# Kernel optimization log

Measured on AMD Instinct MI355X. Metric: run time of the kernel, lower is better.

## Reference

```python
import jax, jax.numpy as jnp
import numpy as np

N_HEADS = 16


def setup_inputs() -> dict:
    key = jax.random.key(0)
    k1, k2, k3, k4 = jax.random.split(key, 4)
    B, W, c, C = 4, 1024, 32, 1024
    x = jax.random.normal(k1, (B, W, c, C), dtype=jnp.float32)
    w_pos_emb = jax.random.normal(k2, (W, C), dtype=jnp.float32)
    attn_w = jax.random.normal(k3, (3 * C, C), dtype=jnp.float32) * (1.0 / np.sqrt(C))
    proj_w = jax.random.normal(k4, (C, C), dtype=jnp.float32) * (1.0 / np.sqrt(C))
    attention_mask = jnp.ones((B, W, c), dtype=jnp.int32)
    return {"x": x, "w_pos_emb": w_pos_emb, "attn_w": attn_w,
            "proj_w": proj_w, "attention_mask": attention_mask}


def reference(x, w_pos_emb, attn_w, proj_w, attention_mask):
    B, W, c, C = x.shape
    H = N_HEADS
    Dh = C // H
    # last-token pooling: one-hot of (count-1) over char axis, multiply-sum
    last_ix = attention_mask.sum(-1) - 1                      # [B, W]
    oh = jax.nn.one_hot(last_ix, c, dtype=x.dtype)            # [B, W, c]
    word = jnp.einsum('bwcd,bwc->bwd', x, oh)                 # [B, W, C]
    word = word + w_pos_emb                                   # first_time pos-emb add
    # QKV projection (torch Linear: y = x @ W^T)
    qkv = jnp.einsum('bwd,ed->bwe', word, attn_w)             # [B, W, 3C]
    q, k, v = jnp.split(qkv, 3, axis=-1)
    def heads(t):
        return t.reshape(B, W, H, Dh).transpose(0, 2, 1, 3)   # [B, H, W, Dh]
    q, k, v = heads(q), heads(k), heads(v)
    scale = 1.0 / np.sqrt(Dh).astype(np.float32)
    scores = jnp.einsum('bhqd,bhkd->bhqk', q, k) * scale      # [B, H, W, W]
    causal = jnp.tril(jnp.ones((W, W), dtype=bool))
    scores = jnp.where(causal, scores, jnp.finfo(scores.dtype).min)
    probs = jax.nn.softmax(scores, axis=-1)
    out = jnp.einsum('bhqk,bhkd->bhqd', probs, v)             # [B, H, W, Dh]
    out = out.transpose(0, 2, 1, 3).reshape(B, W, C)
    out = jnp.einsum('bwd,ed->bwe', out, proj_w)              # c_proj
    # dropout is identity in eval mode
    return (word, out)
```

## Files before the change

kernel.cpp:

```cpp
#include <hip/hip_runtime.h>

#define BB 4
#define WW 1024
#define CDIM 1024
#define CCH 32
#define NH 16
#define DH 64
#define MROWS (BB * WW)

typedef __bf16 bf16x8 __attribute__((ext_vector_type(8)));
typedef float f32x4 __attribute__((ext_vector_type(4)));

static __device__ __forceinline__ unsigned short f2bf(float f) {
    union { float f; unsigned u; } v; v.f = f;
    unsigned r = v.u + 0x7fffu + ((v.u >> 16) & 1u);
    return (unsigned short)(r >> 16);
}

#if defined(__has_builtin)
#if __has_builtin(__builtin_amdgcn_global_load_lds)
#define HAVE_GLL 1
#endif
#endif

#ifdef HAVE_GLL
static __device__ __forceinline__ void gload16(const void* g, void* l) {
    __builtin_amdgcn_global_load_lds(
        (const __attribute__((address_space(1))) unsigned int*)g,
        (__attribute__((address_space(3))) unsigned int*)l, 16, 0, 0);
}
#endif

__global__ __launch_bounds__(256) void prep_kernel(const float* __restrict__ aw,
                                                   const float* __restrict__ pw,
                                                   const float* __restrict__ x,
                                                   const float* __restrict__ pos,
                                                   const int* __restrict__ mask,
                                                   unsigned short* __restrict__ awb,
                                                   unsigned short* __restrict__ pwb,
                                                   float* __restrict__ word_f32,
                                                   unsigned short* __restrict__ word_bf) {
    int blk = blockIdx.x;
    if (blk < 4096) {
        int g = blk * 256 + threadIdx.x;
        const int NA4 = 3 * CDIM * CDIM / 4;
        if (g < NA4) {
            float4 vv = ((const float4*)aw)[g];
            ushort4 o = { f2bf(vv.x), f2bf(vv.y), f2bf(vv.z), f2bf(vv.w) };
            ((ushort4*)awb)[g] = o;
        } else {
            int kk = g - NA4;
            float4 vv = ((const float4*)pw)[kk];
            ushort4 o = { f2bf(vv.x), f2bf(vv.y), f2bf(vv.z), f2bf(vv.w) };
            ((ushort4*)pwb)[kk] = o;
        }
    } else {
        int bw = blk - 4096;
        int w = bw & (WW - 1);
        __shared__ int s_last;
        if (threadIdx.x == 0) {
            int ssum = 0;
            for (int j = 0; j < CCH; ++j) ssum += mask[bw * CCH + j];
            s_last = ssum - 1;
        }
        __syncthreads();
        int last = s_last;
        const float4* xr = (const float4*)(x + ((size_t)bw * CCH + (last < 0 ? 0 : last)) * CDIM);
        const float4* pr = (const float4*)(pos + (size_t)w * CDIM);
        int d4 = threadIdx.x;
        float4 xv = (last >= 0) ? xr[d4] : float4{0.f, 0.f, 0.f, 0.f};
        float4 pv = pr[d4];
        float4 vv = { xv.x + pv.x, xv.y + pv.y, xv.z + pv.z, xv.w + pv.w };
        ((float4*)(word_f32 + (size_t)bw * CDIM))[d4] = vv;
        ushort4 o = { f2bf(vv.x), f2bf(vv.y), f2bf(vv.z), f2bf(vv.w) };
        ((ushort4*)(word_bf + (size_t)bw * CDIM))[d4] = o;
    }
}

template <int EPI, int BM, int BN, int WRN, int WCN, int MI, int NI, int NBX, int CW>
__global__ __launch_bounds__(WRN * WCN * 64) void gemm_nt_kernel(
        const unsigned short* __restrict__ A,
        const unsigned short* __restrict__ Bt,
        int Mdim, int Ndim, int Kdim,
        unsigned short* __restrict__ qb,
        unsigned short* __restrict__ kb,
        unsigned short* __restrict__ vb,
        float* __restrict__ outp) {
    const int NW = WRN * WCN;
    const int NT = NW * 64;
    __shared__ unsigned short As[BM * 64];
    __shared__ unsigned short Bs[BN * 64];
    int t = threadIdx.x;
    int wid = t >> 6, lane = t & 63;
    int wr = wid / WCN, wc = wid % WCN;
    int bid = blockIdx.x;
    int xcd = bid & 7, idx = bid >> 3;
    int bx = xcd * CW + idx % CW;
    int by = idx / CW;
    int mbase = by * BM, nbase = bx * BN;
    int lr = lane & 15, lg = lane >> 4;
    f32x4 acc[MI][NI] = {};

#ifdef HAVE_GLL
    int csrc = ((lane & 7) ^ (lane >> 3)) * 8;
    int rofs = lane >> 3;
    const int TOT = (BM + BN) / 8;
#endif

    for (int kt = 0; kt < Kdim; kt += 64) {
        __syncthreads();
#ifdef HAVE_GLL
        for (int cch = wid; cch < TOT; cch += NW) {
            if (cch < BM / 8)
                gload16(A + (size_t)(mbase + cch * 8 + rofs) * Kdim + kt + csrc, &As[cch * 8 * 64]);
            else {
                int cb = cch - BM / 8;
                gload16(Bt + (size_t)(nbase + cb * 8 + rofs) * Kdim + kt + csrc, &Bs[cb * 8 * 64]);
            }
        }
#else
        for (int s = 0; s < (BM + BN) * 8 / NT; ++s) {
            int f = s * NT + t;
            int row = f >> 3, c8 = (f & 7) * 8;
            if (row < BM)
                *(int4*)&As[row * 64 + (c8 ^ ((row & 7) << 3))] =
                    *(const int4*)&A[(size_t)(mbase + row) * Kdim + kt + c8];
            else {
                int rb = row - BM;
                *(int4*)&Bs[rb * 64 + (c8 ^ ((rb & 7) << 3))] =
                    *(const int4*)&Bt[(size_t)(nbase + rb) * Kdim + kt + c8];
            }
        }
#endif
        __syncthreads();
        for (int ks = 0; ks < 2; ++ks) {
            bf16x8 af[MI], bfr[NI];
            int cc = ks * 32 + lg * 8;
            for (int mi = 0; mi < MI; ++mi) {
                int r = wr * (MI * 16) + mi * 16 + lr;
                af[mi] = *(const bf16x8*)&As[r * 64 + (cc ^ ((r & 7) << 3))];
            }
            for (int ni = 0; ni < NI; ++ni) {
                int r = wc * (NI * 16) + ni * 16 + lr;
                bfr[ni] = *(const bf16x8*)&Bs[r * 64 + (cc ^ ((r & 7) << 3))];
            }
            __builtin_amdgcn_s_setprio(1);
            for (int mi = 0; mi < MI; ++mi)
                for (int ni = 0; ni < NI; ++ni)
                    acc[mi][ni] = __builtin_amdgcn_mfma_f32_16x16x32_bf16(af[mi], bfr[ni], acc[mi][ni], 0, 0, 0);
            __builtin_amdgcn_s_setprio(0);
        }
    }
    for (int mi = 0; mi < MI; ++mi)
        for (int ni = 0; ni < NI; ++ni)
            for (int i = 0; i < 4; ++i) {
                int row = mbase + wr * (MI * 16) + mi * 16 + lg * 4 + i;
                int col = nbase + wc * (NI * 16) + ni * 16 + lr;
                float v = acc[mi][ni][i];
                if (EPI == 0) {
                    int sect = col >> 10, ch = col & 1023, hh = ch >> 6, dd = ch & 63;
                    int bI = row >> 10, wI = row & 1023;
                    size_t dst = ((size_t)(bI * NH + hh) * WW + wI) * DH + dd;
                    if (sect == 0) qb[dst] = f2bf(v * 0.125f);
                    else if (sect == 1) kb[dst] = f2bf(v);
                    else vb[dst] = f2bf(v);
                } else {
                    outp[(size_t)row * Ndim + col] = v;
                }
            }
}

__global__ __launch_bounds__(512) void attn_kernel(const unsigned short* __restrict__ q,
                                                   const unsigned short* __restrict__ k,
                                                   const unsigned short* __restrict__ v,
                                                   unsigned short* __restrict__ aout) {
    __shared__ unsigned short Ks[64 * 64];
    __shared__ unsigned short Vt[64 * 64];
    __shared__ unsigned short Ps0[128 * 64];
    __shared__ unsigned short Ps1[128 * 64];
    int t = threadIdx.x;
    int wid = t >> 6, lane = t & 63;
    int lr = lane & 15, lg = lane >> 4;
    int bid = blockIdx.x;
    int xcd = bid & 7, idx = bid >> 3;
    int bh = xcd + ((idx >> 2) << 3);
    int p = idx & 3;
    int bI = bh >> 4, hI = bh & 15;
    int qa = p * 128, qbv = (7 - p) * 128;
    int nktA = 2 * p + 2, nktB = 16 - 2 * p;
    const float EXP2C = 1.44269504f;
    const float SHIFTC = 28.8539008f;

    bf16x8 qfA[2], qfB[2];
    {
        const unsigned short* qg = q + (size_t)bh * WW * DH;
        int r = wid * 16 + lr;
        for (int ks = 0; ks < 2; ++ks) {
            qfA[ks] = *(const bf16x8*)&qg[(size_t)(qa + r) * DH + ks * 32 + lg * 8];
            qfB[ks] = *(const bf16x8*)&qg[(size_t)(qbv + r) * DH + ks * 32 + lg * 8];
        }
    }

    float rlA[4] = {0.f, 0.f, 0.f, 0.f}, rlB[4] = {0.f, 0.f, 0.f, 0.f};
    f32x4 oA[4] = {}, oB[4] = {};

    const unsigned short* kbase = k + (size_t)bh * WW * DH;
    const unsigned short* vbase = v + (size_t)bh * WW * DH;
    int dp = (t & 31) * 2, kb8 = (t >> 5) & 7;
    int tt = t & 255;
    int krow = tt >> 3, kc8 = (tt & 7) * 8;

    unsigned int vr[8]; int4 kr0, kr1;
    auto prefetch = [&](int tn) {
        if (wid < 4) {
            const unsigned short* vg = vbase + (size_t)tn * 64 * DH;
#pragma unroll
            for (int j = 0; j < 8; ++j)
                vr[j] = *(const unsigned int*)&vg[(size_t)(kb8 * 8 + j) * DH + dp];
        } else {
            const unsigned short* kg = kbase + (size_t)tn * 64 * DH;
            kr0 = *(const int4*)&kg[(size_t)krow * DH + kc8];
            kr1 = *(const int4*)&kg[(size_t)(krow + 32) * DH + kc8];
        }
    };
    prefetch(0);

    auto process = [&](const bf16x8* qf, const bf16x8 (*bfr)[4], int qbase,
                       float* rl, unsigned short* PsX, int tki) {
        f32x4 s[4] = {};
        __builtin_amdgcn_s_setprio(1);
#pragma unroll
        for (int ks = 0; ks < 2; ++ks)
#pragma unroll
            for (int ni = 0; ni < 4; ++ni)
                s[ni] = __builtin_amdgcn_mfma_f32_16x16x32_bf16(qf[ks], bfr[ks][ni], s[ni], 0, 0, 0);
        __builtin_amdgcn_s_setprio(0);
        int rowbase = qbase + wid * 16 + lg * 4;
        if (tki * 64 + 63 > qbase + wid * 16) {
            for (int ni = 0; ni < 4; ++ni)
                for (int i = 0; i < 4; ++i) {
                    int ki = tki * 64 + ni * 16 + lr;
                    if (ki > rowbase + i) s[ni][i] = -1e30f;
                }
        }
#pragma unroll
        for (int ni = 0; ni < 4; ++ni)
#pragma unroll
            for (int i = 0; i < 4; ++i) {
                float pe = __builtin_amdgcn_exp2f(fmaf(s[ni][i], EXP2C, -SHIFTC));
                s[ni][i] = pe;
                rl[i] += pe;
            }
        for (int ni = 0; ni < 4; ++ni)
            for (int i = 0; i < 4; ++i) {
                int r = wid * 16 + lg * 4 + i;
                PsX[r * 64 + ((ni * 16 + lr) ^ ((r & 7) << 3))] = f2bf(s[ni][i]);
            }
    };

    auto pvacc = [&](f32x4* o, const unsigned short* PsX, const bf16x8 (*vbf)[4]) {
#pragma unroll
        for (int ks = 0; ks < 2; ++ks) {
            int cc = ks * 32 + lg * 8;
            int r = wid * 16 + lr;
            bf16x8 pa = *(const bf16x8*)&PsX[r * 64 + (cc ^ ((r & 7) << 3))];
            __builtin_amdgcn_s_setprio(1);
#pragma unroll
            for (int di = 0; di < 4; ++di)
                o[di] = __builtin_amdgcn_mfma_f32_16x16x32_bf16(pa, vbf[ks][di], o[di], 0, 0, 0);
            __builtin_amdgcn_s_setprio(0);
        }
    };

    for (int tki = 0; tki < nktB; ++tki) {
        __syncthreads();
        if (wid < 4) {
            unsigned short lo[8], hi[8];
#pragma unroll
            for (int j = 0; j < 8; ++j) { lo[j] = (unsigned short)(vr[j] & 0xffffu);
                                          hi[j] = (unsigned short)(vr[j] >> 16); }
            *(int4*)&Vt[dp * 64 + ((kb8 * 8) ^ ((dp & 7) << 3))] = *(int4*)lo;
            int d1 = dp + 1;
            *(int4*)&Vt[d1 * 64 + ((kb8 * 8) ^ ((d1 & 7) << 3))] = *(int4*)hi;
        } else {
            *(int4*)&Ks[krow * 64 + (kc8 ^ ((krow & 7) << 3))] = kr0;
            int r1 = krow + 32;
            *(int4*)&Ks[r1 * 64 + (kc8 ^ ((r1 & 7) << 3))] = kr1;
        }
        if (tki + 1 < nktB) prefetch(tki + 1);
        __syncthreads();

        bool wB = (tki * 64 <= qbv + wid * 16 + 15);
        bool wA = (tki < nktA) && (tki * 64 <= qa + wid * 16 + 15);

        bf16x8 bfr[2][4];
#pragma unroll
        for (int ks = 0; ks < 2; ++ks) {
            int cc = ks * 32 + lg * 8;
#pragma unroll
            for (int ni = 0; ni < 4; ++ni) {
                int r = ni * 16 + lr;
                bfr[ks][ni] = *(const bf16x8*)&Ks[r * 64 + (cc ^ ((r & 7) << 3))];
            }
        }
        if (wB) process(qfB, bfr, qbv, rlB, Ps1, tki);
        if (wA) process(qfA, bfr, qa, rlA, Ps0, tki);

        bf16x8 vbf[2][4];
#pragma unroll
        for (int ks = 0; ks < 2; ++ks) {
            int cc = ks * 32 + lg * 8;
#pragma unroll
            for (int di = 0; di < 4; ++di) {
                int rv = di * 16 + lr;
                vbf[ks][di] = *(const bf16x8*)&Vt[rv * 64 + (cc ^ ((rv & 7) << 3))];
            }
        }
        if (wB) pvacc(oB, Ps1, vbf);
        if (wA) pvacc(oA, Ps0, vbf);
    }

    float riA[4], riB[4];
#pragma unroll
    for (int i = 0; i < 4; ++i) {
        for (int d = 8; d >= 1; d >>= 1) rlA[i] += __shfl_xor(rlA[i], d);
        for (int d = 8; d >= 1; d >>= 1) rlB[i] += __shfl_xor(rlB[i], d);
        riA[i] = 1.0f / rlA[i];
        riB[i] = 1.0f / rlB[i];
    }
    for (int di = 0; di < 4; ++di)
        for (int i = 0; i < 4; ++i) {
            int dd = di * 16 + lr;
            int qrA = qa + wid * 16 + lg * 4 + i;
            int qrB = qbv + wid * 16 + lg * 4 + i;
            aout[((size_t)bI * WW + qrA) * CDIM + hI * DH + dd] = f2bf(oA[di][i] * riA[i]);
            aout[((size_t)bI * WW + qrB) * CDIM + hI * DH + dd] = f2bf(oB[di][i] * riB[i]);
        }
}

extern "C" void kernel_launch(void* const* d_in, const int* in_sizes, int n_in,
                              void* d_out, int out_size, void* d_ws, size_t ws_size,
                              hipStream_t stream) {
    const float* x    = (const float*)d_in[0];
    const float* pos  = (const float*)d_in[1];
    const float* aw   = (const float*)d_in[2];
    const float* pw   = (const float*)d_in[3];
    const int*   mask = (const int*)d_in[4];
    float* out = (float*)d_out;
    float* word_f32 = out;
    float* proj_out = out + (size_t)MROWS * CDIM;

    const size_t MB = 1u << 20;
    char* ws = (char*)d_ws;
    unsigned short* word_bf = (unsigned short*)(ws);
    unsigned short* awb     = (unsigned short*)(ws + 8 * MB);
    unsigned short* pwb     = (unsigned short*)(ws + 14 * MB);
    unsigned short* qb      = (unsigned short*)(ws + 16 * MB);
    unsigned short* kb      = (unsigned short*)(ws + 24 * MB);
    unsigned short* vb      = (unsigned short*)(ws + 32 * MB);
    unsigned short* aob     = (unsigned short*)(ws + 40 * MB);

    prep_kernel<<<8192, 256, 0, stream>>>(aw, pw, x, pos, mask, awb, pwb, word_f32, word_bf);
    gemm_nt_kernel<0, 128, 128, 2, 2, 4, 4, 24, 3><<<768, 256, 0, stream>>>(
        word_bf, awb, MROWS, 3 * CDIM, CDIM, qb, kb, vb, nullptr);
    attn_kernel<<<256, 512, 0, stream>>>(qb, kb, vb, aob);
    gemm_nt_kernel<1, 128, 128, 4, 2, 2, 4, 8, 1><<<256, 512, 0, stream>>>(
        aob, pwb, MROWS, CDIM, CDIM, nullptr, nullptr, nullptr, proj_out);
}
```

Baseline: 97.52 us.

## Stage GEMM epilogue through LDS for vectorized stores; retile projection GEMM

After: 98.62 us. About the same (+1.1%).

```diff
diff --git a/kernel.cpp b/kernel.cpp
--- a/kernel.cpp
+++ b/kernel.cpp
@@ -88,8 +88,9 @@
         float* __restrict__ outp) {
     const int NW = WRN * WCN;
     const int NT = NW * 64;
-    __shared__ unsigned short As[BM * 64];
-    __shared__ unsigned short Bs[BN * 64];
+    __shared__ unsigned short SMEM[(BM + BN) * 64];
+    unsigned short* As = SMEM;
+    unsigned short* Bs = SMEM + BM * 64;
     int t = threadIdx.x;
     int wid = t >> 6, lane = t & 63;
     int wr = wid / WCN, wc = wid % WCN;
@@ -151,23 +152,40 @@
             __builtin_amdgcn_s_setprio(0);
         }
     }
-    for (int mi = 0; mi < MI; ++mi)
+
+    const int PITCH = BN + 4;
+    float* Ls = (float*)SMEM;
+    const int CPR = BN / 16;
+    int erow = t / CPR, ech = t % CPR;
+    int grow_base = mbase + (erow >> 4) * (MI * 16) + (erow & 15);
+    __syncthreads();
+    for (int mi = 0; mi < MI; ++mi) {
         for (int ni = 0; ni < NI; ++ni)
-            for (int i = 0; i < 4; ++i) {
-                int row = mbase + wr * (MI * 16) + mi * 16 + lg * 4 + i;
-                int col = nbase + wc * (NI * 16) + ni * 16 + lr;
-                float v = acc[mi][ni][i];
-                if (EPI == 0) {
-                    int sect = col >> 10, ch = col & 1023, hh = ch >> 6, dd = ch & 63;
-                    int bI = row >> 10, wI = row & 1023;
-                    size_t dst = ((size_t)(bI * NH + hh) * WW + wI) * DH + dd;
-                    if (sect == 0) qb[dst] = f2bf(v * 0.125f);
-                    else if (sect == 1) kb[dst] = f2bf(v);
-                    else vb[dst] = f2bf(v);
-                } else {
-                    outp[(size_t)row * Ndim + col] = v;
-                }
-            }
+            for (int i = 0; i < 4; ++i)
+                Ls[(wr * 16 + lg * 4 + i) * PITCH + wc * (NI * 16) + ni * 16 + lr] = acc[mi][ni][i];
+        __syncthreads();
+        float vv[16];
+        for (int j4 = 0; j4 < 4; ++j4)
+            *(float4*)&vv[j4 * 4] = *(const float4*)&Ls[erow * PITCH + ech * 16 + j4 * 4];
+        int grow = grow_base + mi * 16;
+        int gcol = nbase + ech * 16;
+        if (EPI == 0) {
+            int sect = gcol >> 10, hh = (gcol & 1023) >> 6, dd0 = gcol & 63;
+            int bI = grow >> 10, wI = grow & 1023;
+            size_t dst = ((size_t)(bI * NH + hh) * WW + wI) * DH + dd0;
+            float scl = (sect == 0) ? 0.125f : 1.0f;
+            unsigned short ob[16];
+            for (int j = 0; j < 16; ++j) ob[j] = f2bf(vv[j] * scl);
+            unsigned short* bdst = (sect == 0) ? qb : (sect == 1) ? kb : vb;
+            *(int4*)&bdst[dst] = *(const int4*)&ob[0];
+            *(int4*)&bdst[dst + 8] = *(const int4*)&ob[8];
+        } else {
+            float* po = &outp[(size_t)grow * Ndim + gcol];
+            for (int j4 = 0; j4 < 4; ++j4)
+                *(float4*)&po[j4 * 4] = *(const float4*)&vv[j4 * 4];
+        }
+        __syncthreads();
+    }
 }
 
 __global__ __launch_bounds__(512) void attn_kernel(const unsigned short* __restrict__ q,
@@ -364,6 +382,6 @@
     gemm_nt_kernel<0, 128, 128, 2, 2, 4, 4, 24, 3><<<768, 256, 0, stream>>>(
         word_bf, awb, MROWS, 3 * CDIM, CDIM, qb, kb, vb, nullptr);
     attn_kernel<<<256, 512, 0, stream>>>(qb, kb, vb, aob);
-    gemm_nt_kernel<1, 128, 128, 4, 2, 2, 4, 8, 1><<<256, 512, 0, stream>>>(
+    gemm_nt_kernel<1, 128, 64, 4, 1, 2, 4, 16, 2><<<512, 256, 0, stream>>>(
         aob, pwb, MROWS, CDIM, CDIM, nullptr, nullptr, nullptr, proj_out);
 }
```
